# Optimization experiments

Hardware: AMD Instinct MI355X
Metric: run time of the kernel (lower is better)

## Reference

```python
import jax, jax.numpy as jnp
import numpy as np

B, T, QD, KD, E, H, L = 4, 512, 256, 256, 256, 8, 4
DH = E // H
SHAPES = np.array([[64, 64], [32, 32], [16, 16], [8, 8]], dtype=np.int64)
S = int(np.sum(SHAPES[:, 0] * SHAPES[:, 1]))  # 5440


def setup_inputs() -> dict:
    key = jax.random.key(0)
    ks = jax.random.split(key, 16)
    std = 0.02
    return {
        "q": jax.random.normal(ks[0], (B, T, QD), jnp.float32),
        "k": jax.random.normal(ks[1], (B, S, KD), jnp.float32),
        "v": jax.random.normal(ks[2], (B, S, KD), jnp.float32),
        "Wq": jax.random.normal(ks[3], (E, QD), jnp.float32) * std,
        "bq": jnp.zeros((E,), jnp.float32),
        "Wk": jax.random.normal(ks[4], (E, KD), jnp.float32) * std,
        "bk": jnp.zeros((E,), jnp.float32),
        "Wv": jax.random.normal(ks[5], (E, KD), jnp.float32) * std,
        "bv": jnp.zeros((E,), jnp.float32),
        "Wo": jax.random.normal(ks[6], (QD, E), jnp.float32) * std,
        "bo": jnp.zeros((QD,), jnp.float32),
        "Wl": jax.random.normal(ks[7], (H * L, QD), jnp.float32) * std,
        "bl": jnp.zeros((H * L,), jnp.float32),
        "k_spatial_shapes": SHAPES,  # static int metadata (split sizes)
    }


def _heads(x, b):
    # [b, s, E] -> [b, H, s, DH]
    return x.reshape(b, -1, H, DH).transpose(0, 2, 1, 3)


def reference(q, k, v, Wq, bq, Wk, bk, Wv, bv, Wo, bo, Wl, bl, k_spatial_shapes):
    scale = DH ** -0.5
    bsz = q.shape[0]
    # per-head, per-level gate: [B, H, T, L], softmax over levels
    gates = jax.nn.softmax(
        (q @ Wl.T + bl).reshape(bsz, -1, H, L).transpose(0, 2, 1, 3), axis=-1
    )
    qs = _heads((q @ Wq.T + bq) * scale, bsz)   # [B,H,T,DH]
    ks_ = _heads(k @ Wk.T + bk, bsz)            # [B,H,S,DH]
    vs = _heads(v @ Wv.T + bv, bsz)             # [B,H,S,DH]
    scores = jnp.einsum("bhtd,bhsd->bhts", qs, ks_)  # [B,H,T,S]
    sizes = [int(h_ * w_) for h_, w_ in np.asarray(k_spatial_shapes)]
    offs = np.concatenate([[0], np.cumsum(sizes)])
    # segmented softmax per level, weighted by the learned level gate
    pieces = [
        jax.nn.softmax(scores[..., offs[i]:offs[i + 1]], axis=-1) * gates[..., i:i + 1]
        for i in range(len(sizes))
    ]
    attn = jnp.concatenate(pieces, axis=-1)  # [B,H,T,S]
    out = jnp.einsum("bhts,bhsd->bhtd", attn, vs)
    out = out.transpose(0, 2, 1, 3).reshape(bsz, -1, E)
    out = out @ Wo.T + bo
    return out, attn
```

## Files before the change

### kernel.cpp

```cpp
#include <hip/hip_runtime.h>
#include <hip/hip_bf16.h>

#define Bn 4
#define Hn 8
#define Tn 512
#define Sn 5440
#define DHn 32
#define En 256

typedef short bf16x8 __attribute__((ext_vector_type(8)));
typedef float f32x4 __attribute__((ext_vector_type(4)));

static __device__ __forceinline__ unsigned short f2bf(float f) {
    union { float f; unsigned u; } c; c.f = f;
    unsigned r = c.u + 0x7fffu + ((c.u >> 16) & 1u);
    return (unsigned short)(r >> 16);
}

static __device__ __forceinline__ unsigned int cvtpk(float a, float b) {
    __hip_bfloat162 h = __float22bfloat162_rn(make_float2(a, b));
    unsigned int u; __builtin_memcpy(&u, &h, 4); return u;
}

__global__ __launch_bounds__(256) void gates_kernel(
    const float* __restrict__ q, const float* __restrict__ Wl,
    const float* __restrict__ bl, float* __restrict__ gates)
{
    __shared__ float qr[8][256];
    __shared__ float lgs[8][32];
    int tid = threadIdx.x;
    int bt0 = blockIdx.x * 8;

    {
        const float4* src = (const float4*)(q + (size_t)bt0 * 256);
        float4* dst = (float4*)&qr[0][0];
        dst[tid] = src[tid];
        dst[tid + 256] = src[tid + 256];
    }
    __syncthreads();

    int r = tid >> 5, o = tid & 31;
    float acc = 0.f;
    const float4* w4 = (const float4*)(Wl + (size_t)o * 256);
    const float4* q4 = (const float4*)&qr[r][0];
    #pragma unroll 8
    for (int i = 0; i < 64; i++) {
        float4 w = w4[i]; float4 qq = q4[i];
        acc += qq.x*w.x + qq.y*w.y + qq.z*w.z + qq.w*w.w;
    }
    lgs[r][o] = acc + bl[o];
    __syncthreads();

    if (tid < 64) {
        int rr = tid >> 3, h = tid & 7;
        float x0 = lgs[rr][h*4+0], x1 = lgs[rr][h*4+1], x2 = lgs[rr][h*4+2], x3 = lgs[rr][h*4+3];
        float mx = fmaxf(fmaxf(x0,x1), fmaxf(x2,x3));
        float e0 = __expf(x0-mx), e1 = __expf(x1-mx), e2 = __expf(x2-mx), e3 = __expf(x3-mx);
        float inv = 1.f / (e0+e1+e2+e3);
        int bt = bt0 + rr; int b = bt >> 9, t = bt & 511;
        float* g = gates + (((size_t)b*Hn + h)*Tn + t)*4;
        g[0] = e0*inv; g[1] = e1*inv; g[2] = e2*inv; g[3] = e3*inv;
    }
}

static __device__ __forceinline__ void gemm_core(
    const float* __restrict__ A, const float* __restrict__ W,
    int row0, int col0, int tid, int wr, int wc, int lr, int lg,
    unsigned short (*As)[40], unsigned short (*Ws)[40], f32x4 acc[4][4])
{
    for (int k0 = 0; k0 < 256; k0 += 32) {
        __syncthreads();
        #pragma unroll
        for (int i = 0; i < 4; i++) {
            int f4 = tid + i*256;
            int r = f4 >> 3, kc = (f4 & 7) * 4;
            float4 v = *(const float4*)(A + (size_t)(row0 + r)*256 + k0 + kc);
            uint2 pk; pk.x = cvtpk(v.x, v.y); pk.y = cvtpk(v.z, v.w);
            *(uint2*)&As[r][kc] = pk;
        }
        #pragma unroll
        for (int i = 0; i < 4; i++) {
            int f4 = tid + i*256;
            int r = f4 >> 3, kc = (f4 & 7) * 4;
            float4 v = *(const float4*)(W + (size_t)(col0 + r)*256 + k0 + kc);
            uint2 pk; pk.x = cvtpk(v.x, v.y); pk.y = cvtpk(v.z, v.w);
            *(uint2*)&Ws[r][kc] = pk;
        }
        __syncthreads();

        bf16x8 af[4], wf[4];
        #pragma unroll
        for (int i = 0; i < 4; i++) {
            af[i] = *(const bf16x8*)&As[wr*64 + i*16 + lr][lg*8];
            wf[i] = *(const bf16x8*)&Ws[wc*64 + i*16 + lr][lg*8];
        }
        #pragma unroll
        for (int i = 0; i < 4; i++)
            #pragma unroll
            for (int j = 0; j < 4; j++)
                acc[i][j] = __builtin_amdgcn_mfma_f32_16x16x32_bf16(af[i], wf[j], acc[i][j], 0, 0, 0);
    }
}

__global__ __launch_bounds__(256) void proj_kvq(
    const float* __restrict__ kin, const float* __restrict__ Wk, const float* __restrict__ bk,
    const float* __restrict__ vin, const float* __restrict__ Wv, const float* __restrict__ bv,
    const float* __restrict__ qin, const float* __restrict__ Wq, const float* __restrict__ bq,
    unsigned short* __restrict__ ks_out, unsigned short* __restrict__ vt_out,
    unsigned short* __restrict__ qs_out)
{
    int mode = blockIdx.z;
    if (mode == 2 && blockIdx.x >= 16) return;

    __shared__ unsigned short As[128][40];
    __shared__ unsigned short Ws[128][40];

    const float* A    = (mode == 0) ? kin : (mode == 1) ? vin : qin;
    const float* W    = (mode == 0) ? Wk  : (mode == 1) ? Wv  : Wq;
    const float* bias = (mode == 0) ? bk  : (mode == 1) ? bv  : bq;

    int tid = threadIdx.x;
    int l = tid & 63, wid = tid >> 6;
    int wr = wid >> 1, wc = wid & 1;
    int lr = l & 15, lg = l >> 4;
    int row0 = blockIdx.x * 128, col0 = blockIdx.y * 128;

    f32x4 acc[4][4] = {};
    gemm_core(A, W, row0, col0, tid, wr, wc, lr, lg, As, Ws, acc);

    const float qscale = 0.17677669529663687f * 1.4426950408889634f;

    #pragma unroll
    for (int i = 0; i < 4; i++) {
        int m0 = row0 + wr*64 + i*16 + lg*4;
        #pragma unroll
        for (int j = 0; j < 4; j++) {
            int col = col0 + wc*64 + j*16 + lr;
            float bvv = bias[col];
            if (mode == 0) {
                #pragma unroll
                for (int r = 0; r < 4; r++) {
                    int m = m0 + r;
                    int b = m / Sn, s = m - b*Sn;
                    ks_out[(((size_t)b*Hn + (col >> 5))*Sn + s)*DHn + (col & 31)] = f2bf(acc[i][j][r] + bvv);
                }
            } else if (mode == 1) {
                int b = m0 / Sn, s0 = m0 - b*Sn;
                uint2 pk;
                pk.x = cvtpk(acc[i][j][0] + bvv, acc[i][j][1] + bvv);
                pk.y = cvtpk(acc[i][j][2] + bvv, acc[i][j][3] + bvv);
                *(uint2*)&vt_out[(((size_t)b*Hn + (col >> 5))*DHn + (col & 31))*Sn + s0] = pk;
            } else {
                #pragma unroll
                for (int r = 0; r < 4; r++) {
                    int m = m0 + r;
                    int b = m >> 9, t = m & 511;
                    qs_out[(((size_t)b*Hn + (col >> 5))*Tn + t)*DHn + (col & 31)] = f2bf((acc[i][j][r] + bvv) * qscale);
                }
            }
        }
    }
}

__global__ __launch_bounds__(256) void proj_out(
    const float* __restrict__ A, const float* __restrict__ W,
    const float* __restrict__ bias, float* __restrict__ out)
{
    __shared__ unsigned short As[128][40];
    __shared__ unsigned short Ws[128][40];

    int tid = threadIdx.x;
    int l = tid & 63, wid = tid >> 6;
    int wr = wid >> 1, wc = wid & 1;
    int lr = l & 15, lg = l >> 4;
    int row0 = blockIdx.x * 128, col0 = blockIdx.y * 128;

    f32x4 acc[4][4] = {};
    gemm_core(A, W, row0, col0, tid, wr, wc, lr, lg, As, Ws, acc);

    #pragma unroll
    for (int i = 0; i < 4; i++) {
        int m0 = row0 + wr*64 + i*16 + lg*4;
        #pragma unroll
        for (int j = 0; j < 4; j++) {
            int col = col0 + wc*64 + j*16 + lr;
            float bvv = bias[col];
            #pragma unroll
            for (int r = 0; r < 4; r++)
                __builtin_nontemporal_store(acc[i][j][r] + bvv, &out[(size_t)(m0 + r)*256 + col]);
        }
    }
}

__global__ __launch_bounds__(256) void attn_fused(
    const unsigned short* __restrict__ qs, const unsigned short* __restrict__ ks,
    const unsigned short* __restrict__ vt, const float* __restrict__ gates,
    float* __restrict__ attn_out, float* __restrict__ o_tmp)
{
    __shared__ char plds[4][2048];
    __shared__ char estw[4][4096];
    __shared__ float lsum[4][4][16];
    __shared__ float denom[4][16];
    __shared__ float outred[4][16][32];

    int n = blockIdx.x;
    int bh = ((n >> 8) << 3) | (n & 7);
    int tt = (n >> 3) & 31;
    int t0 = tt << 4;
    int b = bh >> 3, h = bh & 7;
    int tid = threadIdx.x;
    int l = tid & 63, w = tid >> 6;
    int lr = l & 15, lg = l >> 4;

    bf16x8 aq = *(const bf16x8*)(qs + ((size_t)bh*Tn + t0 + lr)*DHn + lg*8);
    const unsigned short* kb = ks + (size_t)bh * Sn * DHn;
    const unsigned short* vb = vt + (size_t)bh * DHn * Sn;
    const f32x4 fzero = {0.f, 0.f, 0.f, 0.f};

    float lp0 = 0.f, lp1 = 0.f, lp2 = 0.f, lp3 = 0.f;
    bf16x8 kf0, kf1, kf2, kf3;
    {
        const unsigned short* kc_ = kb + (size_t)w * 64 * DHn;
        kf0 = *(const bf16x8*)(kc_ + (size_t)(lr     )*DHn + lg*8);
        kf1 = *(const bf16x8*)(kc_ + (size_t)(16 + lr)*DHn + lg*8);
        kf2 = *(const bf16x8*)(kc_ + (size_t)(32 + lr)*DHn + lg*8);
        kf3 = *(const bf16x8*)(kc_ + (size_t)(48 + lr)*DHn + lg*8);
    }
    for (int c = w; c < 85; c += 4) {
        bf16x8 kn0, kn1, kn2, kn3;
        int cn = c + 4;
        if (cn < 85) {
            const unsigned short* kc_ = kb + (size_t)cn * 64 * DHn;
            kn0 = *(const bf16x8*)(kc_ + (size_t)(lr     )*DHn + lg*8);
            kn1 = *(const bf16x8*)(kc_ + (size_t)(16 + lr)*DHn + lg*8);
            kn2 = *(const bf16x8*)(kc_ + (size_t)(32 + lr)*DHn + lg*8);
            kn3 = *(const bf16x8*)(kc_ + (size_t)(48 + lr)*DHn + lg*8);
        }
        __builtin_amdgcn_s_setprio(1);
        f32x4 s0 = __builtin_amdgcn_mfma_f32_16x16x32_bf16(kf0, aq, fzero, 0, 0, 0);
        f32x4 s1 = __builtin_amdgcn_mfma_f32_16x16x32_bf16(kf1, aq, fzero, 0, 0, 0);
        f32x4 s2 = __builtin_amdgcn_mfma_f32_16x16x32_bf16(kf2, aq, fzero, 0, 0, 0);
        f32x4 s3 = __builtin_amdgcn_mfma_f32_16x16x32_bf16(kf3, aq, fzero, 0, 0, 0);
        __builtin_amdgcn_s_setprio(0);
        float es = exp2f(s0[0]) + exp2f(s0[1]) + exp2f(s0[2]) + exp2f(s0[3])
                 + exp2f(s1[0]) + exp2f(s1[1]) + exp2f(s1[2]) + exp2f(s1[3])
                 + exp2f(s2[0]) + exp2f(s2[1]) + exp2f(s2[2]) + exp2f(s2[3])
                 + exp2f(s3[0]) + exp2f(s3[1]) + exp2f(s3[2]) + exp2f(s3[3]);
        if      (c < 64) lp0 += es;
        else if (c < 80) lp1 += es;
        else if (c < 84) lp2 += es;
        else             lp3 += es;
        kf0 = kn0; kf1 = kn1; kf2 = kn2; kf3 = kn3;
    }
    {
        float v;
        v = lp0; v += __shfl_xor(v, 16); v += __shfl_xor(v, 32); lp0 = v;
        v = lp1; v += __shfl_xor(v, 16); v += __shfl_xor(v, 32); lp1 = v;
        v = lp2; v += __shfl_xor(v, 16); v += __shfl_xor(v, 32); lp2 = v;
        v = lp3; v += __shfl_xor(v, 16); v += __shfl_xor(v, 32); lp3 = v;
    }
    if (l < 16) {
        lsum[w][0][lr] = lp0; lsum[w][1][lr] = lp1;
        lsum[w][2][lr] = lp2; lsum[w][3][lr] = lp3;
    }
    __syncthreads();
    if (tid < 64) {
        int seg = tid >> 4, row = tid & 15;
        denom[seg][row] = lsum[0][seg][row] + lsum[1][seg][row] + lsum[2][seg][row] + lsum[3][seg][row];
    }
    __syncthreads();

    float cf0, cf1, cf2, cf3;
    {
        const float* g = gates + ((size_t)bh*Tn + t0 + lr)*4;
        cf0 = g[0] / denom[0][lr];
        cf1 = g[1] / denom[1][lr];
        cf2 = g[2] / denom[2][lr];
        cf3 = g[3] / denom[3][lr];
    }

    f32x4 acc0 = fzero, acc1 = fzero;
    char* pbase = plds[w];
    char* ebase = estw[w];
    int swz = (lr & 7) << 4;
    float* abase = attn_out + ((size_t)bh*Tn + t0)*Sn;

    bf16x8 vf0, vf1, vf2, vf3;
    {
        const unsigned short* kc_ = kb + (size_t)w * 64 * DHn;
        kf0 = *(const bf16x8*)(kc_ + (size_t)(lr     )*DHn + lg*8);
        kf1 = *(const bf16x8*)(kc_ + (size_t)(16 + lr)*DHn + lg*8);
        kf2 = *(const bf16x8*)(kc_ + (size_t)(32 + lr)*DHn + lg*8);
        kf3 = *(const bf16x8*)(kc_ + (size_t)(48 + lr)*DHn + lg*8);
        vf0 = *(const bf16x8*)(vb + (size_t)(lr     )*Sn + w*64      + lg*8);
        vf1 = *(const bf16x8*)(vb + (size_t)(16 + lr)*Sn + w*64      + lg*8);
        vf2 = *(const bf16x8*)(vb + (size_t)(lr     )*Sn + w*64 + 32 + lg*8);
        vf3 = *(const bf16x8*)(vb + (size_t)(16 + lr)*Sn + w*64 + 32 + lg*8);
    }

    for (int c = w; c < 85; c += 4) {
        bf16x8 kn0, kn1, kn2, kn3, vn0, vn1, vn2, vn3;
        int cn = c + 4;
        if (cn < 85) {
            const unsigned short* kc_ = kb + (size_t)cn * 64 * DHn;
            kn0 = *(const bf16x8*)(kc_ + (size_t)(lr     )*DHn + lg*8);
            kn1 = *(const bf16x8*)(kc_ + (size_t)(16 + lr)*DHn + lg*8);
            kn2 = *(const bf16x8*)(kc_ + (size_t)(32 + lr)*DHn + lg*8);
            kn3 = *(const bf16x8*)(kc_ + (size_t)(48 + lr)*DHn + lg*8);
            vn0 = *(const bf16x8*)(vb + (size_t)(lr     )*Sn + cn*64      + lg*8);
            vn1 = *(const bf16x8*)(vb + (size_t)(16 + lr)*Sn + cn*64      + lg*8);
            vn2 = *(const bf16x8*)(vb + (size_t)(lr     )*Sn + cn*64 + 32 + lg*8);
            vn3 = *(const bf16x8*)(vb + (size_t)(16 + lr)*Sn + cn*64 + 32 + lg*8);
        }
        float cf = (c < 64) ? cf0 : (c < 80) ? cf1 : (c < 84) ? cf2 : cf3;

        __builtin_amdgcn_s_setprio(1);
        f32x4 s0 = __builtin_amdgcn_mfma_f32_16x16x32_bf16(kf0, aq, fzero, 0, 0, 0);
        f32x4 s1 = __builtin_amdgcn_mfma_f32_16x16x32_bf16(kf1, aq, fzero, 0, 0, 0);
        f32x4 s2 = __builtin_amdgcn_mfma_f32_16x16x32_bf16(kf2, aq, fzero, 0, 0, 0);
        f32x4 s3 = __builtin_amdgcn_mfma_f32_16x16x32_bf16(kf3, aq, fzero, 0, 0, 0);
        __builtin_amdgcn_s_setprio(0);

        {
            f32x4 av;
            av[0] = exp2f(s0[0])*cf; av[1] = exp2f(s0[1])*cf; av[2] = exp2f(s0[2])*cf; av[3] = exp2f(s0[3])*cf;
            *(f32x4*)(ebase + ((lr*256 +   0 + lg*16) ^ swz));
            *(f32x4*)(ebase + ((lr*256 +   0 + lg*16) ^ swz)) = av;
            uint2 pk; pk.x = cvtpk(av[0], av[1]); pk.y = cvtpk(av[2], av[3]);
            *(uint2*)(pbase + ((lr*128 +   0 + lg*8) ^ swz)) = pk;
            av[0] = exp2f(s1[0])*cf; av[1] = exp2f(s1[1])*cf; av[2] = exp2f(s1[2])*cf; av[3] = exp2f(s1[3])*cf;
            *(f32x4*)(ebase + ((lr*256 +  64 + lg*16) ^ swz)) = av;
            pk.x = cvtpk(av[0], av[1]); pk.y = cvtpk(av[2], av[3]);
            *(uint2*)(pbase + ((lr*128 +  32 + lg*8) ^ swz)) = pk;
            av[0] = exp2f(s2[0])*cf; av[1] = exp2f(s2[1])*cf; av[2] = exp2f(s2[2])*cf; av[3] = exp2f(s2[3])*cf;
            *(f32x4*)(ebase + ((lr*256 + 128 + lg*16) ^ swz)) = av;
            pk.x = cvtpk(av[0], av[1]); pk.y = cvtpk(av[2], av[3]);
            *(uint2*)(pbase + ((lr*128 +  64 + lg*8) ^ swz)) = pk;
            av[0] = exp2f(s3[0])*cf; av[1] = exp2f(s3[1])*cf; av[2] = exp2f(s3[2])*cf; av[3] = exp2f(s3[3])*cf;
            *(f32x4*)(ebase + ((lr*256 + 192 + lg*16) ^ swz)) = av;
            pk.x = cvtpk(av[0], av[1]); pk.y = cvtpk(av[2], av[3]);
            *(uint2*)(pbase + ((lr*128 +  96 + lg*8) ^ swz)) = pk;
        }

        __builtin_amdgcn_s_setprio(1);
        {
            bf16x8 pa0 = *(const bf16x8*)(pbase + ((lr*128 +      lg*16) ^ swz));
            acc0 = __builtin_amdgcn_mfma_f32_16x16x32_bf16(pa0, vf0, acc0, 0, 0, 0);
            acc1 = __builtin_amdgcn_mfma_f32_16x16x32_bf16(pa0, vf1, acc1, 0, 0, 0);
            bf16x8 pa1 = *(const bf16x8*)(pbase + ((lr*128 + 64 + lg*16) ^ swz));
            acc0 = __builtin_amdgcn_mfma_f32_16x16x32_bf16(pa1, vf2, acc0, 0, 0, 0);
            acc1 = __builtin_amdgcn_mfma_f32_16x16x32_bf16(pa1, vf3, acc1, 0, 0, 0);
        }
        __builtin_amdgcn_s_setprio(0);

        #pragma unroll
        for (int i = 0; i < 4; i++) {
            int row = i*4 + lg;
            f32x4 vv = *(const f32x4*)(ebase + ((row*256 + lr*16) ^ ((row & 7) << 4)));
            __builtin_nontemporal_store(vv, (f32x4*)(abase + (size_t)row*Sn + c*64 + lr*4));
        }

        kf0 = kn0; kf1 = kn1; kf2 = kn2; kf3 = kn3;
        vf0 = vn0; vf1 = vn1; vf2 = vn2; vf3 = vn3;
    }

    #pragma unroll
    for (int r = 0; r < 4; r++) {
        outred[w][4*lg + r][lr]      = acc0[r];
        outred[w][4*lg + r][16 + lr] = acc1[r];
    }
    __syncthreads();
    #pragma unroll
    for (int i = 0; i < 2; i++) {
        int idx = tid + i*256;
        int row = idx >> 5, d = idx & 31;
        float sum = outred[0][row][d] + outred[1][row][d] + outred[2][row][d] + outred[3][row][d];
        __builtin_nontemporal_store(sum, &o_tmp[((size_t)(b*Tn + t0 + row))*En + h*DHn + d]);
    }
}

extern "C" void kernel_launch(void* const* d_in, const int* in_sizes, int n_in,
                              void* d_out, int out_size, void* d_ws, size_t ws_size,
                              hipStream_t stream)
{
    const float* q  = (const float*)d_in[0];
    const float* k  = (const float*)d_in[1];
    const float* v  = (const float*)d_in[2];
    const float* Wq = (const float*)d_in[3];
    const float* bq = (const float*)d_in[4];
    const float* Wk = (const float*)d_in[5];
    const float* bk = (const float*)d_in[6];
    const float* Wv = (const float*)d_in[7];
    const float* bv = (const float*)d_in[8];
    const float* Wo = (const float*)d_in[9];
    const float* bo = (const float*)d_in[10];
    const float* Wl = (const float*)d_in[11];
    const float* bl = (const float*)d_in[12];

    float* out  = (float*)d_out;
    float* attn = out + (size_t)Bn*Tn*256;

    char* ws = (char*)d_ws;
    unsigned short* qs    = (unsigned short*)ws;
    unsigned short* ksb   = (unsigned short*)(ws + (1u<<20));
    unsigned short* vtb   = (unsigned short*)(ws + (1u<<20) + 11141120u);
    float*          gates = (float*)(ws + (1u<<20) + 2u*11141120u);
    float*          o_tmp = (float*)(ws + (1u<<20) + 2u*11141120u + 262144u);

    gates_kernel<<<Bn*Tn/8, 256, 0, stream>>>(q, Wl, bl, gates);
    proj_kvq<<<dim3((Bn*Sn)/128, 2, 3), 256, 0, stream>>>(
        k, Wk, bk, v, Wv, bv, q, Wq, bq, ksb, vtb, qs);
    attn_fused<<<Bn*Hn*(Tn/16), 256, 0, stream>>>(qs, ksb, vtb, gates, attn, o_tmp);
    proj_out<<<dim3((Bn*Tn)/128, 2), 256, 0, stream>>>(o_tmp, Wo, bo, out);
}
```

Baseline: 159.7 us.

## Drop register prefetch of K/V, remove setprio, fold gate scale into exp2

Removes the manual software prefetch of the next K and V fragments in both passes, so each chunk's loads are now issued inside the loop right before use. This lowers register pressure and could raise occupancy, but it exposes global load latency unless other waves hide it. It also removes the s_setprio hints around the MFMAs. The per-level gate/denominator factor is moved into the exponent as a log2 add, replacing a multiply per element with an add, and the fast __log2f slightly changes precision.

```diff
diff --git a/kernel.cpp b/kernel.cpp
--- a/kernel.cpp
+++ b/kernel.cpp
@@ -218,30 +218,16 @@
     const f32x4 fzero = {0.f, 0.f, 0.f, 0.f};
 
     float lp0 = 0.f, lp1 = 0.f, lp2 = 0.f, lp3 = 0.f;
-    bf16x8 kf0, kf1, kf2, kf3;
-    {
-        const unsigned short* kc_ = kb + (size_t)w * 64 * DHn;
-        kf0 = *(const bf16x8*)(kc_ + (size_t)(lr     )*DHn + lg*8);
-        kf1 = *(const bf16x8*)(kc_ + (size_t)(16 + lr)*DHn + lg*8);
-        kf2 = *(const bf16x8*)(kc_ + (size_t)(32 + lr)*DHn + lg*8);
-        kf3 = *(const bf16x8*)(kc_ + (size_t)(48 + lr)*DHn + lg*8);
-    }
     for (int c = w; c < 85; c += 4) {
-        bf16x8 kn0, kn1, kn2, kn3;
-        int cn = c + 4;
-        if (cn < 85) {
-            const unsigned short* kc_ = kb + (size_t)cn * 64 * DHn;
-            kn0 = *(const bf16x8*)(kc_ + (size_t)(lr     )*DHn + lg*8);
-            kn1 = *(const bf16x8*)(kc_ + (size_t)(16 + lr)*DHn + lg*8);
-            kn2 = *(const bf16x8*)(kc_ + (size_t)(32 + lr)*DHn + lg*8);
-            kn3 = *(const bf16x8*)(kc_ + (size_t)(48 + lr)*DHn + lg*8);
-        }
-        __builtin_amdgcn_s_setprio(1);
+        const unsigned short* kc_ = kb + (size_t)c * 64 * DHn;
+        bf16x8 kf0 = *(const bf16x8*)(kc_ + (size_t)(lr     )*DHn + lg*8);
+        bf16x8 kf1 = *(const bf16x8*)(kc_ + (size_t)(16 + lr)*DHn + lg*8);
+        bf16x8 kf2 = *(const bf16x8*)(kc_ + (size_t)(32 + lr)*DHn + lg*8);
+        bf16x8 kf3 = *(const bf16x8*)(kc_ + (size_t)(48 + lr)*DHn + lg*8);
         f32x4 s0 = __builtin_amdgcn_mfma_f32_16x16x32_bf16(kf0, aq, fzero, 0, 0, 0);
         f32x4 s1 = __builtin_amdgcn_mfma_f32_16x16x32_bf16(kf1, aq, fzero, 0, 0, 0);
         f32x4 s2 = __builtin_amdgcn_mfma_f32_16x16x32_bf16(kf2, aq, fzero, 0, 0, 0);
         f32x4 s3 = __builtin_amdgcn_mfma_f32_16x16x32_bf16(kf3, aq, fzero, 0, 0, 0);
-        __builtin_amdgcn_s_setprio(0);
         float es = exp2f(s0[0]) + exp2f(s0[1]) + exp2f(s0[2]) + exp2f(s0[3])
                  + exp2f(s1[0]) + exp2f(s1[1]) + exp2f(s1[2]) + exp2f(s1[3])
                  + exp2f(s2[0]) + exp2f(s2[1]) + exp2f(s2[2]) + exp2f(s2[3])
@@ -250,7 +236,6 @@
         else if (c < 80) lp1 += es;
         else if (c < 84) lp2 += es;
         else             lp3 += es;
-        kf0 = kn0; kf1 = kn1; kf2 = kn2; kf3 = kn3;
     }
     {
         float v;
@@ -270,13 +255,13 @@
     }
     __syncthreads();
 
-    float cf0, cf1, cf2, cf3;
+    float lcf0, lcf1, lcf2, lcf3;
     {
         const float* g = gates + ((size_t)bh*Tn + t0 + lr)*4;
-        cf0 = g[0] / denom[0][lr];
-        cf1 = g[1] / denom[1][lr];
-        cf2 = g[2] / denom[2][lr];
-        cf3 = g[3] / denom[3][lr];
+        lcf0 = __log2f(g[0] / denom[0][lr]);
+        lcf1 = __log2f(g[1] / denom[1][lr]);
+        lcf2 = __log2f(g[2] / denom[2][lr]);
+        lcf3 = __log2f(g[3] / denom[3][lr]);
     }
 
     f32x4 acc0 = fzero, acc1 = fzero;
@@ -285,58 +270,39 @@
     int swz = (lr & 7) << 4;
     float* abase = attn_out + ((size_t)bh*Tn + t0)*Sn;
 
-    bf16x8 vf0, vf1, vf2, vf3;
-    {
-        const unsigned short* kc_ = kb + (size_t)w * 64 * DHn;
-        kf0 = *(const bf16x8*)(kc_ + (size_t)(lr     )*DHn + lg*8);
-        kf1 = *(const bf16x8*)(kc_ + (size_t)(16 + lr)*DHn + lg*8);
-        kf2 = *(const bf16x8*)(kc_ + (size_t)(32 + lr)*DHn + lg*8);
-        kf3 = *(const bf16x8*)(kc_ + (size_t)(48 + lr)*DHn + lg*8);
-        vf0 = *(const bf16x8*)(vb + (size_t)(lr     )*Sn + w*64      + lg*8);
-        vf1 = *(const bf16x8*)(vb + (size_t)(16 + lr)*Sn + w*64      + lg*8);
-        vf2 = *(const bf16x8*)(vb + (size_t)(lr     )*Sn + w*64 + 32 + lg*8);
-        vf3 = *(const bf16x8*)(vb + (size_t)(16 + lr)*Sn + w*64 + 32 + lg*8);
-    }
-
     for (int c = w; c < 85; c += 4) {
-        bf16x8 kn0, kn1, kn2, kn3, vn0, vn1, vn2, vn3;
-        int cn = c + 4;
-        if (cn < 85) {
-            const unsigned short* kc_ = kb + (size_t)cn * 64 * DHn;
-            kn0 = *(const bf16x8*)(kc_ + (size_t)(lr     )*DHn + lg*8);
-            kn1 = *(const bf16x8*)(kc_ + (size_t)(16 + lr)*DHn + lg*8);
-            kn2 = *(const bf16x8*)(kc_ + (size_t)(32 + lr)*DHn + lg*8);
-            kn3 = *(const bf16x8*)(kc_ + (size_t)(48 + lr)*DHn + lg*8);
-            vn0 = *(const bf16x8*)(vb + (size_t)(lr     )*Sn + cn*64      + lg*8);
-            vn1 = *(const bf16x8*)(vb + (size_t)(16 + lr)*Sn + cn*64      + lg*8);
-            vn2 = *(const bf16x8*)(vb + (size_t)(lr     )*Sn + cn*64 + 32 + lg*8);
-            vn3 = *(const bf16x8*)(vb + (size_t)(16 + lr)*Sn + cn*64 + 32 + lg*8);
-        }
-        float cf = (c < 64) ? cf0 : (c < 80) ? cf1 : (c < 84) ? cf2 : cf3;
-
-        __builtin_amdgcn_s_setprio(1);
+        float lcf = (c < 64) ? lcf0 : (c < 80) ? lcf1 : (c < 84) ? lcf2 : lcf3;
+
+        const unsigned short* kc_ = kb + (size_t)c * 64 * DHn;
+        bf16x8 kf0 = *(const bf16x8*)(kc_ + (size_t)(lr     )*DHn + lg*8);
+        bf16x8 kf1 = *(const bf16x8*)(kc_ + (size_t)(16 + lr)*DHn + lg*8);
+        bf16x8 kf2 = *(const bf16x8*)(kc_ + (size_t)(32 + lr)*DHn + lg*8);
+        bf16x8 kf3 = *(const bf16x8*)(kc_ + (size_t)(48 + lr)*DHn + lg*8);
+        bf16x8 vf0 = *(const bf16x8*)(vb + (size_t)(lr     )*Sn + c*64      + lg*8);
+        bf16x8 vf1 = *(const bf16x8*)(vb + (size_t)(16 + lr)*Sn + c*64      + lg*8);
+        bf16x8 vf2 = *(const bf16x8*)(vb + (size_t)(lr     )*Sn + c*64 + 32 + lg*8);
+        bf16x8 vf3 = *(const bf16x8*)(vb + (size_t)(16 + lr)*Sn + c*64 + 32 + lg*8);
+
         f32x4 s0 = __builtin_amdgcn_mfma_f32_16x16x32_bf16(kf0, aq, fzero, 0, 0, 0);
         f32x4 s1 = __builtin_amdgcn_mfma_f32_16x16x32_bf16(kf1, aq, fzero, 0, 0, 0);
         f32x4 s2 = __builtin_amdgcn_mfma_f32_16x16x32_bf16(kf2, aq, fzero, 0, 0, 0);
         f32x4 s3 = __builtin_amdgcn_mfma_f32_16x16x32_bf16(kf3, aq, fzero, 0, 0, 0);
-        __builtin_amdgcn_s_setprio(0);
 
         {
             f32x4 av;
-            av[0] = exp2f(s0[0])*cf; av[1] = exp2f(s0[1])*cf; av[2] = exp2f(s0[2])*cf; av[3] = exp2f(s0[3])*cf;
-            *(f32x4*)(ebase + ((lr*256 +   0 + lg*16) ^ swz));
+            av[0] = exp2f(s0[0]+lcf); av[1] = exp2f(s0[1]+lcf); av[2] = exp2f(s0[2]+lcf); av[3] = exp2f(s0[3]+lcf);
             *(f32x4*)(ebase + ((lr*256 +   0 + lg*16) ^ swz)) = av;
             uint2 pk; pk.x = cvtpk(av[0], av[1]); pk.y = cvtpk(av[2], av[3]);
             *(uint2*)(pbase + ((lr*128 +   0 + lg*8) ^ swz)) = pk;
-            av[0] = exp2f(s1[0])*cf; av[1] = exp2f(s1[1])*cf; av[2] = exp2f(s1[2])*cf; av[3] = exp2f(s1[3])*cf;
+            av[0] = exp2f(s1[0]+lcf); av[1] = exp2f(s1[1]+lcf); av[2] = exp2f(s1[2]+lcf); av[3] = exp2f(s1[3]+lcf);
             *(f32x4*)(ebase + ((lr*256 +  64 + lg*16) ^ swz)) = av;
             pk.x = cvtpk(av[0], av[1]); pk.y = cvtpk(av[2], av[3]);
             *(uint2*)(pbase + ((lr*128 +  32 + lg*8) ^ swz)) = pk;
-            av[0] = exp2f(s2[0])*cf; av[1] = exp2f(s2[1])*cf; av[2] = exp2f(s2[2])*cf; av[3] = exp2f(s2[3])*cf;
+            av[0] = exp2f(s2[0]+lcf); av[1] = exp2f(s2[1]+lcf); av[2] = exp2f(s2[2]+lcf); av[3] = exp2f(s2[3]+lcf);
             *(f32x4*)(ebase + ((lr*256 + 128 + lg*16) ^ swz)) = av;
             pk.x = cvtpk(av[0], av[1]); pk.y = cvtpk(av[2], av[3]);
             *(uint2*)(pbase + ((lr*128 +  64 + lg*8) ^ swz)) = pk;
-            av[0] = exp2f(s3[0])*cf; av[1] = exp2f(s3[1])*cf; av[2] = exp2f(s3[2])*cf; av[3] = exp2f(s3[3])*cf;
+            av[0] = exp2f(s3[0]+lcf); av[1] = exp2f(s3[1]+lcf); av[2] = exp2f(s3[2]+lcf); av[3] = exp2f(s3[3]+lcf);
             *(f32x4*)(ebase + ((lr*256 + 192 + lg*16) ^ swz)) = av;
             pk.x = cvtpk(av[0], av[1]); pk.y = cvtpk(av[2], av[3]);
             *(uint2*)(pbase + ((lr*128 +  96 + lg*8) ^ swz)) = pk;
@@ -359,9 +325,6 @@
             f32x4 vv = *(const f32x4*)(ebase + ((row*256 + lr*16) ^ ((row & 7) << 4)));
             __builtin_nontemporal_store(vv, (f32x4*)(abase + (size_t)row*Sn + c*64 + lr*4));
         }
-
-        kf0 = kn0; kf1 = kn1; kf2 = kn2; kf3 = kn3;
-        vf0 = vn0; vf1 = vn1; vf2 = vn2; vf3 = vn3;
     }
 
     #pragma unroll
```

After: 158.3 us. About the same (-0.9%).
